# Kernel optimization log

Hardware: AMD Instinct MI355X
Metric: run time of the kernel (lower is better)

## Reference

```python
import jax, jax.numpy as jnp
import numpy as np

E, D_IN, D_OUT, A, R, T = 8, 1024, 1024, 4, 16, 8192


def setup_inputs() -> dict:
    key = jax.random.key(0)
    ks = jax.random.split(key, 6)
    x = jax.random.normal(ks[0], (T, D_IN), jnp.float32)
    weight = jax.random.normal(ks[1], (E, D_IN, D_OUT), jnp.float32) / np.float32(np.sqrt(D_IN))
    # he_uniform-like scale for lora_A; lora_B random (zeros in real init would hide the LoRA path)
    lora_A = jax.random.normal(ks[2], (A, E, D_IN, R), jnp.float32) * np.float32(np.sqrt(2.0 / D_IN))
    lora_B = jax.random.normal(ks[3], (A, E, R, D_OUT), jnp.float32) * np.float32(0.02)
    lora_scaling = jax.random.uniform(ks[4], (A,), jnp.float32, 0.5, 1.5)
    group_sizes = jnp.full((E,), T // E, dtype=jnp.int32)  # sums to T
    adapter_indices_sorted = jax.random.randint(ks[5], (T,), 0, A, dtype=jnp.int32)
    return {
        'x': x, 'weight': weight, 'lora_A': lora_A, 'lora_B': lora_B,
        'lora_scaling': lora_scaling, 'group_sizes': group_sizes,
        'adapter_indices_sorted': adapter_indices_sorted,
    }


def reference(x, weight, lora_A, lora_B, lora_scaling, group_sizes, adapter_indices_sorted):
    total_tokens, d_in = x.shape
    n_experts, _, d_out = weight.shape
    n_adapters, _, _, rank = lora_A.shape
    n_groups = n_adapters * n_experts

    # Base expert-grouped GEMM: x is already sorted by expert via group_sizes.
    base_out = jax.lax.ragged_dot(x, weight, group_sizes)  # [T, d_out]

    # Combined (adapter, expert) group id per token.
    expert_idx = jnp.repeat(jnp.arange(n_experts), group_sizes, total_repeat_length=total_tokens)
    flat_idx = adapter_indices_sorted * n_experts + expert_idx  # [T]

    # prepare_routing: stable sort tokens by combined group id.
    sort_idx = jnp.argsort(flat_idx, stable=True)
    x_sorted = x[sort_idx]
    combined_group_sizes = jnp.zeros((n_groups,), jnp.int32).at[flat_idx].add(1)
    unsort_idx = jnp.argsort(sort_idx)

    # Nested LoRA grouped GEMMs over flattened (adapter, expert) groups.
    lora_A_flat = lora_A.reshape(n_groups, d_in, rank)
    lora_B_flat = lora_B.reshape(n_groups, rank, d_out)
    intermediate = jax.lax.ragged_dot(x_sorted, lora_A_flat, combined_group_sizes)  # [T, rank]
    lora_out_sorted = jax.lax.ragged_dot(intermediate, lora_B_flat, combined_group_sizes)  # [T, d_out]

    lora_out = lora_out_sorted[unsort_idx] * lora_scaling[adapter_indices_sorted, None]
    return base_out + lora_out
```

## Files before the change

### kernel.cpp

```cpp
#include <hip/hip_runtime.h>
#include <hip/hip_bf16.h>
#include <stdint.h>


#define T_TOK 8192
#define DIN   1024
#define DOUT  1024
#define NE    8
#define NA    4
#define RK    16
#define KEXT  1088
#define NOCT  136

typedef __attribute__((ext_vector_type(8))) short short8;
typedef __attribute__((ext_vector_type(4))) float f32x4;

__device__ __forceinline__ ushort f2bf(float f) {
  union { float f; uint32_t i; } v; v.f = f;
  uint32_t x = v.i;
  return (ushort)((x + 0x7fffu + ((x >> 16) & 1u)) >> 16);
}

__device__ __forceinline__ void gload_lds16(const void* g, void* l) {
  __builtin_amdgcn_global_load_lds(
      (const __attribute__((address_space(1))) uint32_t*)g,
      (__attribute__((address_space(3))) uint32_t*)l,
      16, 0, 0);
}

__device__ __forceinline__ int expert_of_row(const int* __restrict__ gs, int row) {
  int cum = 0, e = 0;
#pragma unroll
  for (int i = 0; i < NE; ++i) { if (row >= cum) e = i; cum += gs[i]; }
  return e;
}

__global__ __launch_bounds__(256) void k_prep(
    const float* __restrict__ x, const float* __restrict__ weight,
    const float* __restrict__ lora_A, const float* __restrict__ lora_B,
    const float* __restrict__ lora_scaling,
    ushort* __restrict__ xp, ushort* __restrict__ Aoct, ushort* __restrict__ Boct) {
  const int bid = blockIdx.x;
  const int tid = threadIdx.x;

  if (bid < 8192) {
    int idx = bid * 256 + tid;
    int row = idx >> 8;
    int c4 = idx & 255;
    float4 v = *(const float4*)(x + (size_t)row * DIN + c4 * 4);
    ushort4 b;
    b.x = f2bf(v.x); b.y = f2bf(v.y); b.z = f2bf(v.z); b.w = f2bf(v.w);
    *(ushort4*)(xp + (size_t)row * KEXT + c4 * 4) = b;
  } else if (bid < 8448) {
    int u = (bid - 8192) * 4 + (tid >> 6);
    int e = u >> 7, ko = u & 127;
    int c = tid & 63;
    int a = c >> 4, r = c & 15;
    float s = lora_scaling[a];
    ushort o8[8];
#pragma unroll
    for (int j = 0; j < 8; ++j) {
      float v = lora_A[((size_t)(a * NE + e) * DIN + ko * 8 + j) * RK + r];
      o8[j] = f2bf(s * v);
    }
    *(uint4*)(Aoct + ((size_t)((e * 128 + ko) * 64 + c)) * 8) = *(const uint4*)o8;
  } else {
    int e, ko;
    const float* srcbase;
    int stride;
    if (bid < 9472) {
      int u = bid - 8448;
      e = u >> 7; ko = u & 127;
      srcbase = weight + (size_t)e * DIN * DOUT + (size_t)(ko * 8) * DOUT;
      stride = DOUT;
    } else {
      int u = bid - 9472;
      e = u >> 3; int o = u & 7; ko = 128 + o;
      srcbase = nullptr; stride = 0;
    }
    int n4 = tid * 4;
    float v[8][4];
    if (bid < 9472) {
#pragma unroll
      for (int j = 0; j < 8; ++j) {
        float4 q = *(const float4*)(srcbase + (size_t)j * stride + n4);
        v[j][0] = q.x; v[j][1] = q.y; v[j][2] = q.z; v[j][3] = q.w;
      }
    } else {
      int o = ko - 128;
#pragma unroll
      for (int j = 0; j < 8; ++j) {
        int kv = o * 8 + j;
        int a = kv >> 4, r = kv & 15;
        float4 q = *(const float4*)(lora_B + (size_t)((a * NE + e) * RK + r) * DOUT + n4);
        v[j][0] = q.x; v[j][1] = q.y; v[j][2] = q.z; v[j][3] = q.w;
      }
    }
    ushort* dst = Boct + ((size_t)(e * NOCT + ko) * DOUT + n4) * 8;
#pragma unroll
    for (int i = 0; i < 4; ++i) {
      ushort o8[8];
#pragma unroll
      for (int j = 0; j < 8; ++j) o8[j] = f2bf(v[j][i]);
      *(uint4*)(dst + i * 8) = *(const uint4*)o8;
    }
  }
}

__global__ __launch_bounds__(256) void k_vA(
    ushort* __restrict__ xp, const ushort* __restrict__ Aoct,
    const int* __restrict__ gs, const int* __restrict__ adapter_idx) {
  __shared__ ushort As2[64 * 64];
  __shared__ ushort Bs2[8 * 64 * 8];

  const int tid = threadIdx.x;
  const int lane = tid & 63;
  const int wave = tid >> 6;
  const int rows0 = blockIdx.x * 64;
  const int e = expert_of_row(gs, rows0);
  const ushort* aoct = Aoct + (size_t)e * 128 * 64 * 8;

  f32x4 acc[4];
#pragma unroll
  for (int ni = 0; ni < 4; ++ni) acc[ni] = (f32x4){0.f, 0.f, 0.f, 0.f};

  const int r8 = lane >> 3;
  const int c8s = (lane & 7) ^ r8;

  for (int kt = 0; kt < 16; ++kt) {
#pragma unroll
    for (int rd = 0; rd < 2; ++rd) {
      int row = wave * 16 + rd * 8 + r8;
      const ushort* src = xp + (size_t)(rows0 + row) * KEXT + kt * 64 + c8s * 8;
      gload_lds16(src, &As2[(wave * 16 + rd * 8) * 64]);
    }
#pragma unroll
    for (int rd = 0; rd < 2; ++rd) {
      int o = wave * 2 + rd;
      const ushort* src = aoct + ((size_t)(kt * 8 + o) * 64 + lane) * 8;
      gload_lds16(src, &Bs2[o * 64 * 8]);
    }
    __syncthreads();

    int m = wave * 16 + (lane & 15);
#pragma unroll
    for (int h = 0; h < 2; ++h) {
      int kblk = h * 4 + (lane >> 4);
      short8 af = *(const short8*)&As2[m * 64 + (kblk ^ (m & 7)) * 8];
#pragma unroll
      for (int ni = 0; ni < 4; ++ni) {
        short8 bfv = *(const short8*)&Bs2[(kblk * 64 + ni * 16 + (lane & 15)) * 8];
        acc[ni] = __builtin_amdgcn_mfma_f32_16x16x32_bf16(af, bfv, acc[ni], 0, 0, 0);
      }
    }
    __syncthreads();
  }

#pragma unroll
  for (int i = 0; i < 4; ++i) {
    int grow = rows0 + wave * 16 + (lane >> 4) * 4 + i;
    int a_row = adapter_idx[grow];
#pragma unroll
    for (int ni = 0; ni < 4; ++ni) {
      float val = (a_row == ni) ? acc[ni][i] : 0.f;
      xp[(size_t)grow * KEXT + DIN + ni * 16 + (lane & 15)] = f2bf(val);
    }
  }
}

__global__ __launch_bounds__(256) void k_gemm(
    const ushort* __restrict__ xp, const ushort* __restrict__ Boct,
    const int* __restrict__ gs, float* __restrict__ out) {
  __shared__ ushort As[128 * 64];
  __shared__ ushort Bs[8 * 128 * 8];

  const int tid = threadIdx.x;
  const int lane = tid & 63;
  const int wave = tid >> 6;
  const int wm = wave >> 1, wn = wave & 1;

  const int row0 = blockIdx.y * 128;
  const int n0 = blockIdx.x * 128;
  const int e = expert_of_row(gs, row0);
  const ushort* boct = Boct + (size_t)e * NOCT * DOUT * 8;

  f32x4 acc[4][4];
#pragma unroll
  for (int mi = 0; mi < 4; ++mi)
#pragma unroll
    for (int ni = 0; ni < 4; ++ni) acc[mi][ni] = (f32x4){0.f, 0.f, 0.f, 0.f};

  const int r8 = lane >> 3;
  const int c8s = (lane & 7) ^ r8;

  for (int kt = 0; kt < 17; ++kt) {
#pragma unroll
    for (int rd = 0; rd < 4; ++rd) {
      int row = wave * 32 + rd * 8 + r8;
      const ushort* src = xp + (size_t)(row0 + row) * KEXT + kt * 64 + c8s * 8;
      gload_lds16(src, &As[(wave * 32 + rd * 8) * 64]);
    }
#pragma unroll
    for (int rd = 0; rd < 4; ++rd) {
      int u = wave * 4 + rd;
      int o = u >> 1, hf = u & 1;
      const ushort* src = boct + ((size_t)(kt * 8 + o) * DOUT + n0 + hf * 64 + lane) * 8;
      gload_lds16(src, &Bs[(o * 128 + hf * 64) * 8]);
    }
    __syncthreads();

#pragma unroll
    for (int h = 0; h < 2; ++h) {
      int kblk = h * 4 + (lane >> 4);
      short8 af[4], bfv[4];
#pragma unroll
      for (int mi = 0; mi < 4; ++mi) {
        int m = wm * 64 + mi * 16 + (lane & 15);
        af[mi] = *(const short8*)&As[m * 64 + (kblk ^ (m & 7)) * 8];
      }
#pragma unroll
      for (int ni = 0; ni < 4; ++ni) {
        int n = wn * 64 + ni * 16 + (lane & 15);
        bfv[ni] = *(const short8*)&Bs[(kblk * 128 + n) * 8];
      }
#pragma unroll
      for (int mi = 0; mi < 4; ++mi)
#pragma unroll
        for (int ni = 0; ni < 4; ++ni)
          acc[mi][ni] = __builtin_amdgcn_mfma_f32_16x16x32_bf16(
              af[mi], bfv[ni], acc[mi][ni], 0, 0, 0);
    }
    __syncthreads();
  }

#pragma unroll
  for (int mi = 0; mi < 4; ++mi) {
#pragma unroll
    for (int ni = 0; ni < 4; ++ni) {
      int col = n0 + wn * 64 + ni * 16 + (lane & 15);
#pragma unroll
      for (int i = 0; i < 4; ++i) {
        int row = row0 + wm * 64 + mi * 16 + (lane >> 4) * 4 + i;
        out[(size_t)row * DOUT + col] = acc[mi][ni][i];
      }
    }
  }
}

extern "C" void kernel_launch(void* const* d_in, const int* in_sizes, int n_in,
                              void* d_out, int out_size, void* d_ws, size_t ws_size,
                              hipStream_t stream) {
  const float* x            = (const float*)d_in[0];
  const float* weight       = (const float*)d_in[1];
  const float* lora_A       = (const float*)d_in[2];
  const float* lora_B       = (const float*)d_in[3];
  const float* lora_scaling = (const float*)d_in[4];
  const int*   group_sizes  = (const int*)d_in[5];
  const int*   adapter_idx  = (const int*)d_in[6];
  float* out = (float*)d_out;

  const size_t sz_xp    = (size_t)T_TOK * KEXT * 2;
  const size_t sz_boct  = (size_t)NE * NOCT * DOUT * 8 * 2;
  ushort* xp   = (ushort*)d_ws;
  ushort* boct = (ushort*)((char*)d_ws + sz_xp);
  ushort* aoct = (ushort*)((char*)d_ws + sz_xp + sz_boct);

  k_prep<<<9536, 256, 0, stream>>>(x, weight, lora_A, lora_B, lora_scaling,
                                   xp, aoct, boct);
  k_vA<<<T_TOK / 64, 256, 0, stream>>>(xp, aoct, group_sizes, adapter_idx);
  dim3 grid(DOUT / 128, T_TOK / 128);
  k_gemm<<<grid, 256, 0, stream>>>(xp, boct, group_sizes, out);
}
```

Baseline: 164.0 us.

## Fuse x bf16 conversion into LoRA-A kernel and swizzle GEMM block order

Moves the fp32-to-bf16 conversion of x out of the prep kernel and into the LoRA-A projection kernel. Each block converts its x tile, writes it to the padded bf16 buffer for the main GEMM, and also stores it straight into shared memory, so the separate pass that re-reads bf16 x is gone. The main GEMM switches to a 1D grid with a swizzled block-to-tile mapping, which changes the order tiles are scheduled in and so their cache locality. The cost is that x loads in the LoRA-A kernel are now synchronous register loads rather than async LDS loads.

```diff
diff --git a/kernel.cpp b/kernel.cpp
--- a/kernel.cpp
+++ b/kernel.cpp
@@ -36,23 +36,15 @@
 }
 
 __global__ __launch_bounds__(256) void k_prep(
-    const float* __restrict__ x, const float* __restrict__ weight,
+    const float* __restrict__ weight,
     const float* __restrict__ lora_A, const float* __restrict__ lora_B,
     const float* __restrict__ lora_scaling,
-    ushort* __restrict__ xp, ushort* __restrict__ Aoct, ushort* __restrict__ Boct) {
+    ushort* __restrict__ Aoct, ushort* __restrict__ Boct) {
   const int bid = blockIdx.x;
   const int tid = threadIdx.x;
 
-  if (bid < 8192) {
-    int idx = bid * 256 + tid;
-    int row = idx >> 8;
-    int c4 = idx & 255;
-    float4 v = *(const float4*)(x + (size_t)row * DIN + c4 * 4);
-    ushort4 b;
-    b.x = f2bf(v.x); b.y = f2bf(v.y); b.z = f2bf(v.z); b.w = f2bf(v.w);
-    *(ushort4*)(xp + (size_t)row * KEXT + c4 * 4) = b;
-  } else if (bid < 8448) {
-    int u = (bid - 8192) * 4 + (tid >> 6);
+  if (bid < 256) {
+    int u = bid * 4 + (tid >> 6);
     int e = u >> 7, ko = u & 127;
     int c = tid & 63;
     int a = c >> 4, r = c & 15;
@@ -68,19 +60,19 @@
     int e, ko;
     const float* srcbase;
     int stride;
-    if (bid < 9472) {
-      int u = bid - 8448;
+    if (bid < 1280) {
+      int u = bid - 256;
       e = u >> 7; ko = u & 127;
       srcbase = weight + (size_t)e * DIN * DOUT + (size_t)(ko * 8) * DOUT;
       stride = DOUT;
     } else {
-      int u = bid - 9472;
+      int u = bid - 1280;
       e = u >> 3; int o = u & 7; ko = 128 + o;
       srcbase = nullptr; stride = 0;
     }
     int n4 = tid * 4;
     float v[8][4];
-    if (bid < 9472) {
+    if (bid < 1280) {
 #pragma unroll
       for (int j = 0; j < 8; ++j) {
         float4 q = *(const float4*)(srcbase + (size_t)j * stride + n4);
@@ -107,8 +99,9 @@
   }
 }
 
-__global__ __launch_bounds__(256) void k_vA(
-    ushort* __restrict__ xp, const ushort* __restrict__ Aoct,
+__global__ __launch_bounds__(256) void k_xva(
+    const float* __restrict__ x, ushort* __restrict__ xp,
+    const ushort* __restrict__ Aoct,
     const int* __restrict__ gs, const int* __restrict__ adapter_idx) {
   __shared__ ushort As2[64 * 64];
   __shared__ ushort Bs2[8 * 64 * 8];
@@ -120,26 +113,41 @@
   const int e = expert_of_row(gs, rows0);
   const ushort* aoct = Aoct + (size_t)e * 128 * 64 * 8;
 
+  const int row = tid >> 2;
+  const int seg = tid & 3;
+  const int r7 = row & 7;
+  const int c0 = seg * 2;
+
   f32x4 acc[4];
 #pragma unroll
   for (int ni = 0; ni < 4; ++ni) acc[ni] = (f32x4){0.f, 0.f, 0.f, 0.f};
 
-  const int r8 = lane >> 3;
-  const int c8s = (lane & 7) ^ r8;
-
   for (int kt = 0; kt < 16; ++kt) {
-#pragma unroll
-    for (int rd = 0; rd < 2; ++rd) {
-      int row = wave * 16 + rd * 8 + r8;
-      const ushort* src = xp + (size_t)(rows0 + row) * KEXT + kt * 64 + c8s * 8;
-      gload_lds16(src, &As2[(wave * 16 + rd * 8) * 64]);
-    }
 #pragma unroll
     for (int rd = 0; rd < 2; ++rd) {
       int o = wave * 2 + rd;
       const ushort* src = aoct + ((size_t)(kt * 8 + o) * 64 + lane) * 8;
       gload_lds16(src, &Bs2[o * 64 * 8]);
     }
+
+    const float* srcx = x + (size_t)(rows0 + row) * DIN + kt * 64 + seg * 16;
+    float4 q0 = ((const float4*)srcx)[0];
+    float4 q1 = ((const float4*)srcx)[1];
+    float4 q2 = ((const float4*)srcx)[2];
+    float4 q3 = ((const float4*)srcx)[3];
+    ushort o16[16];
+    o16[0] = f2bf(q0.x); o16[1] = f2bf(q0.y); o16[2] = f2bf(q0.z); o16[3] = f2bf(q0.w);
+    o16[4] = f2bf(q1.x); o16[5] = f2bf(q1.y); o16[6] = f2bf(q1.z); o16[7] = f2bf(q1.w);
+    o16[8]  = f2bf(q2.x); o16[9]  = f2bf(q2.y); o16[10] = f2bf(q2.z); o16[11] = f2bf(q2.w);
+    o16[12] = f2bf(q3.x); o16[13] = f2bf(q3.y); o16[14] = f2bf(q3.z); o16[15] = f2bf(q3.w);
+
+    ushort* dstg = xp + (size_t)(rows0 + row) * KEXT + kt * 64 + seg * 16;
+    *(uint4*)(dstg)     = ((const uint4*)o16)[0];
+    *(uint4*)(dstg + 8) = ((const uint4*)o16)[1];
+
+    *(uint4*)&As2[row * 64 + ((c0 ^ r7) * 8)]       = ((const uint4*)o16)[0];
+    *(uint4*)&As2[row * 64 + (((c0 + 1) ^ r7) * 8)] = ((const uint4*)o16)[1];
+
     __syncthreads();
 
     int m = wave * 16 + (lane & 15);
@@ -179,8 +187,10 @@
   const int wave = tid >> 6;
   const int wm = wave >> 1, wn = wave & 1;
 
-  const int row0 = blockIdx.y * 128;
-  const int n0 = blockIdx.x * 128;
+  const int bid = blockIdx.x;
+  const int swz = (bid & 7) * 64 + (bid >> 3);
+  const int row0 = (swz >> 3) * 128;
+  const int n0 = (swz & 7) * 128;
   const int e = expert_of_row(gs, row0);
   const ushort* boct = Boct + (size_t)e * NOCT * DOUT * 8;
 
@@ -196,8 +206,8 @@
   for (int kt = 0; kt < 17; ++kt) {
 #pragma unroll
     for (int rd = 0; rd < 4; ++rd) {
-      int row = wave * 32 + rd * 8 + r8;
-      const ushort* src = xp + (size_t)(row0 + row) * KEXT + kt * 64 + c8s * 8;
+      int r = wave * 32 + rd * 8 + r8;
+      const ushort* src = xp + (size_t)(row0 + r) * KEXT + kt * 64 + c8s * 8;
       gload_lds16(src, &As[(wave * 32 + rd * 8) * 64]);
     }
 #pragma unroll
@@ -240,8 +250,8 @@
       int col = n0 + wn * 64 + ni * 16 + (lane & 15);
 #pragma unroll
       for (int i = 0; i < 4; ++i) {
-        int row = row0 + wm * 64 + mi * 16 + (lane >> 4) * 4 + i;
-        out[(size_t)row * DOUT + col] = acc[mi][ni][i];
+        int r = row0 + wm * 64 + mi * 16 + (lane >> 4) * 4 + i;
+        out[(size_t)r * DOUT + col] = acc[mi][ni][i];
       }
     }
   }
@@ -265,9 +275,8 @@
   ushort* boct = (ushort*)((char*)d_ws + sz_xp);
   ushort* aoct = (ushort*)((char*)d_ws + sz_xp + sz_boct);
 
-  k_prep<<<9536, 256, 0, stream>>>(x, weight, lora_A, lora_B, lora_scaling,
-                                   xp, aoct, boct);
-  k_vA<<<T_TOK / 64, 256, 0, stream>>>(xp, aoct, group_sizes, adapter_idx);
-  dim3 grid(DOUT / 128, T_TOK / 128);
-  k_gemm<<<grid, 256, 0, stream>>>(xp, boct, group_sizes, out);
-}
+  k_prep<<<1344, 256, 0, stream>>>(weight, lora_A, lora_B, lora_scaling,
+                                   aoct, boct);
+  k_xva<<<T_TOK / 64, 256, 0, stream>>>(x, xp, aoct, group_sizes, adapter_idx);
+  k_gemm<<<512, 256, 0, stream>>>(xp, boct, group_sizes, out);
+}
```

New measurement: 162.5 us. Within noise of the previous version (-0.9%).
